# Performance work log

Measured on AMD Instinct MI355X. Metric: run time of the kernel, lower is better.

The kernel has to match this reference:

```python
import jax, jax.numpy as jnp
import numpy as np

EMB = 1024
HEADS = 16
HEAD_DIM = EMB // HEADS


def setup_inputs() -> dict:
    key = jax.random.key(0)
    ks = jax.random.split(key, 9)
    B, T = 2, 2048
    s = 1.0 / np.sqrt(EMB)
    x = jax.random.normal(ks[0], (B, T, EMB), dtype=jnp.float32)
    Wq = jax.random.normal(ks[1], (EMB, EMB), dtype=jnp.float32) * s
    bq = jnp.zeros((EMB,), dtype=jnp.float32)
    Wk = jax.random.normal(ks[2], (EMB, EMB), dtype=jnp.float32) * s
    bk = jnp.zeros((EMB,), dtype=jnp.float32)
    Wv = jax.random.normal(ks[3], (EMB, EMB), dtype=jnp.float32) * s
    bv = jnp.zeros((EMB,), dtype=jnp.float32)
    Wo = jax.random.normal(ks[4], (EMB, EMB), dtype=jnp.float32) * s
    bo = jnp.zeros((EMB,), dtype=jnp.float32)
    return {"x": x, "Wq": Wq, "bq": bq, "Wk": Wk, "bk": bk,
            "Wv": Wv, "bv": bv, "Wo": Wo, "bo": bo}


def reference(x, Wq, bq, Wk, bk, Wv, bv, Wo, bo):
    B, T, C = x.shape
    H, D = HEADS, HEAD_DIM
    # QKV projections -> (B, H, T, D)
    q = (x @ Wq + bq).reshape(B, T, H, D).transpose(0, 2, 1, 3)
    k = (x @ Wk + bk).reshape(B, T, H, D).transpose(0, 2, 1, 3)
    v = (x @ Wv + bv).reshape(B, T, H, D).transpose(0, 2, 1, 3)
    scores = jnp.einsum('bhqd,bhkd->bhqk', q, k) / np.sqrt(D).astype(np.float32)
    causal = jnp.tril(jnp.ones((T, T), dtype=bool))  # True where allowed
    scores = jnp.where(causal, scores, -jnp.inf)
    weights = jax.nn.softmax(scores, axis=-1)  # dropout is identity at eval
    out = jnp.einsum('bhqk,bhkd->bhqd', weights, v)
    out = out.transpose(0, 2, 1, 3).reshape(B, T, C)
    return out @ Wo + bo
```

## Files before the change

### kernel.cpp

```cpp
#include <hip/hip_runtime.h>

typedef unsigned short u16;
typedef u16 u16x8 __attribute__((ext_vector_type(8)));
typedef __bf16 bf16x8 __attribute__((ext_vector_type(8)));
typedef float f32x4 __attribute__((ext_vector_type(4)));

#define EMB 1024
#define TT 2048
#define BB 2
#define NHEADS 16
#define HD 64
#define MTOT (BB * TT)

__device__ __forceinline__ u16 cvt(float f) {
  return __builtin_bit_cast(u16, (__bf16)f);
}

__device__ __forceinline__ bf16x8 asbf(u16x8 v) {
  return __builtin_bit_cast(bf16x8, v);
}

__device__ __forceinline__ void gload16(const void* g, void* l) {
  __builtin_amdgcn_global_load_lds(
      (const __attribute__((address_space(1))) void*)g,
      (__attribute__((address_space(3))) void*)l, 16, 0, 0);
}

__global__ __launch_bounds__(256) void k_prep(
    const float* __restrict__ x, u16* __restrict__ xb,
    const float* __restrict__ W0, const float* __restrict__ W1,
    const float* __restrict__ W2, const float* __restrict__ W3,
    u16* __restrict__ T0, u16* __restrict__ T1, u16* __restrict__ T2,
    u16* __restrict__ T3) {
  __shared__ float tile[32][33];
  const int bid = blockIdx.x;
  const int tid = threadIdx.x;
  if (bid >= 4096) {
    int i = (bid - 4096) * 256 + tid;
    float4 a = ((const float4*)x)[i * 2];
    float4 b = ((const float4*)x)[i * 2 + 1];
    u16x8 o;
    o[0] = cvt(a.x); o[1] = cvt(a.y); o[2] = cvt(a.z); o[3] = cvt(a.w);
    o[4] = cvt(b.x); o[5] = cvt(b.y); o[6] = cvt(b.z); o[7] = cvt(b.w);
    ((u16x8*)xb)[i] = o;
    return;
  }
  const int z = bid >> 10;
  const float* __restrict__ W = (z == 0) ? W0 : (z == 1) ? W1 : (z == 2) ? W2 : W3;
  u16* __restrict__ Wt = (z == 0) ? T0 : (z == 1) ? T1 : (z == 2) ? T2 : T3;
  const int b = bid & 1023;
  const int bx = (b & 31) * 32, by = (b >> 5) * 32;
  const int tx = tid & 31;
  const int ty = tid >> 5;
#pragma unroll
  for (int r = ty; r < 32; r += 8) tile[r][tx] = W[(by + r) * EMB + bx + tx];
  __syncthreads();
  const int tx2 = tid & 15;
  const int ty2 = tid >> 4;
#pragma unroll
  for (int r = ty2; r < 32; r += 16) {
    unsigned v = (unsigned)cvt(tile[2 * tx2][r]) |
                 ((unsigned)cvt(tile[2 * tx2 + 1][r]) << 16);
    *(unsigned*)&Wt[(bx + r) * EMB + by + 2 * tx2] = v;
  }
}

__global__ __launch_bounds__(256) void k_gemm_qkv(
    const u16* __restrict__ xb, const u16* __restrict__ WqT,
    const u16* __restrict__ WkT, const u16* __restrict__ WvT,
    const float* __restrict__ bq, const float* __restrict__ bk,
    const float* __restrict__ bv, u16* __restrict__ Q, u16* __restrict__ K,
    u16* __restrict__ Vt) {
  __shared__ u16 WS[4][2][2][2048];
  const int tid = threadIdx.x;
  const int lane = tid & 63;
  const int w = tid >> 6;
  const int wr = w >> 1, wc = w & 1;
  const int lr = lane & 15, lg = lane >> 4;
  const int m0 = blockIdx.x * 128;
  const int nb = blockIdx.y;
  const int seg = nb >> 3;
  const int n0 = (nb & 7) * 128;
  const u16* __restrict__ Bt = (seg == 0) ? WqT : (seg == 1) ? WkT : WvT;
  const float* __restrict__ bias = (seg == 0) ? bq : (seg == 1) ? bk : bv;

  f32x4 acc[4][4];
#pragma unroll
  for (int i = 0; i < 4; i++)
#pragma unroll
    for (int j = 0; j < 4; j++) acc[i][j] = (f32x4){0.f, 0.f, 0.f, 0.f};

  const int srow = lane >> 2;
  const int sc = (lane & 3) ^ ((lane >> 3) & 3);
  const u16* gA = xb + (m0 + wr * 64 + srow) * EMB + sc * 8;
  const u16* gB = Bt + (n0 + wc * 64 + srow) * EMB + sc * 8;
  char* wbase = (char*)WS + w * 16384;
  const int pc = (lg ^ ((lr >> 1) & 3)) * 16;

#pragma unroll
  for (int j = 0; j < 4; j++) {
    gload16(gA + j * 16 * EMB, wbase + j * 1024);
    gload16(gB + j * 16 * EMB, wbase + 4096 + j * 1024);
  }

  for (int k0 = 0; k0 < EMB; k0 += 32) {
    const int cur = (k0 >> 5) & 1;
    char* bcur = wbase + cur * 8192;
    if (k0 + 32 < EMB) {
      char* bnxt = wbase + (cur ^ 1) * 8192;
      const int kn = k0 + 32;
#pragma unroll
      for (int j = 0; j < 4; j++) {
        gload16(gA + j * 16 * EMB + kn, bnxt + j * 1024);
        gload16(gB + j * 16 * EMB + kn, bnxt + 4096 + j * 1024);
      }
      asm volatile("s_waitcnt vmcnt(8)" ::: "memory");
    } else {
      asm volatile("s_waitcnt vmcnt(0)" ::: "memory");
    }
    __builtin_amdgcn_sched_barrier(0);
    u16x8 af[4], bf[4];
#pragma unroll
    for (int mi = 0; mi < 4; mi++)
      af[mi] = *(const u16x8*)(bcur + (mi * 16 + lr) * 64 + pc);
#pragma unroll
    for (int ni = 0; ni < 4; ni++)
      bf[ni] = *(const u16x8*)(bcur + 4096 + (ni * 16 + lr) * 64 + pc);
    __builtin_amdgcn_s_setprio(1);
#pragma unroll
    for (int mi = 0; mi < 4; mi++)
#pragma unroll
      for (int ni = 0; ni < 4; ni++)
        acc[mi][ni] = __builtin_amdgcn_mfma_f32_16x16x32_bf16(
            asbf(af[mi]), asbf(bf[ni]), acc[mi][ni], 0, 0, 0);
    __builtin_amdgcn_s_setprio(0);
  }

  const int b = m0 >> 11;
  if (seg == 2) {
#pragma unroll
    for (int ni = 0; ni < 4; ni++) {
      const int n = n0 + wc * 64 + ni * 16 + lr;
      const float bv_ = bias[n];
      const int h = n >> 6, d = n & 63;
      u16* vrow = Vt + (((b * NHEADS + h) * HD) + d) * TT;
#pragma unroll
      for (int mi = 0; mi < 4; mi++) {
        const int t0 = (m0 + wr * 64 + mi * 16 + lg * 4) & 2047;
        ushort4 pk;
        pk.x = cvt(acc[mi][ni][0] + bv_);
        pk.y = cvt(acc[mi][ni][1] + bv_);
        pk.z = cvt(acc[mi][ni][2] + bv_);
        pk.w = cvt(acc[mi][ni][3] + bv_);
        *(ushort4*)&vrow[t0] = pk;
      }
    }
  } else {
    u16* __restrict__ dst = (seg == 0) ? Q : K;
    const float qs = (seg == 0) ? 0.18033688011f : 1.0f;
#pragma unroll
    for (int mi = 0; mi < 4; mi++) {
      const int lmb = wr * 64 + mi * 16 + lg * 4;
#pragma unroll
      for (int ni = 0; ni < 4; ni++) {
        const int n = n0 + wc * 64 + ni * 16 + lr;
        const float bv_ = bias[n];
        const int h = n >> 6, d = n & 63;
#pragma unroll
        for (int r = 0; r < 4; r++) {
          const int t = (m0 + lmb + r) & 2047;
          float v = (acc[mi][ni][r] + bv_) * qs;
          dst[(((b * NHEADS + h) * TT) + t) * HD + d] = cvt(v);
        }
      }
    }
  }
}

__global__ __launch_bounds__(512) void k_attn(const u16* __restrict__ Q,
                                              const u16* __restrict__ Kg,
                                              const u16* __restrict__ Vt,
                                              u16* __restrict__ AO) {
  __shared__ u16 Kl[2][64 * 64];
  __shared__ u16 Vl[2][64 * 64];
  const int tid = threadIdx.x;
  const int lane = tid & 63;
  const int w = tid >> 6;
  const int lr = lane & 15, lg = lane >> 4;
  const int bh = blockIdx.x;
  const int pair = blockIdx.y;
  const int lo = pair, hi = 31 - pair;
  const int qblk = (w < 4) ? hi : lo;
  const int myend = qblk;
  const int q0 = qblk * 64 + (w & 3) * 16;
  const u16* __restrict__ Qh = Q + bh * TT * HD;
  const u16* __restrict__ Kh = Kg + bh * TT * HD;
  const u16* __restrict__ Vh = Vt + bh * HD * TT;

  const int srow = tid >> 3;
  const int sgz = ((tid >> 3) & 3) | (((tid >> 6) & 1) << 2);
  const int sc = (tid & 7) ^ sgz;

  u16x8 qf[2];
  qf[0] = *(const u16x8*)&Qh[(q0 + lr) * HD + lg * 8];
  qf[1] = *(const u16x8*)&Qh[(q0 + lr) * HD + 32 + lg * 8];

  f32x4 accO[4];
#pragma unroll
  for (int i = 0; i < 4; i++) accO[i] = (f32x4){0.f, 0.f, 0.f, 0.f};
  float mst = -__builtin_inff();
  float lsum = 0.f;

  const int nkt = hi + 1;

  gload16(Kh + srow * HD + sc * 8, (char*)Kl[0] + w * 1024);
  gload16(Vh + srow * TT + sc * 8, (char*)Vl[0] + w * 1024);
  __syncthreads();

  for (int kt = 0; kt < nkt; ++kt) {
    const int k0 = kt * 64;
    const int cur = kt & 1;
    if (kt + 1 < nkt) {
      const int kn = k0 + 64;
      gload16(Kh + (kn + srow) * HD + sc * 8, (char*)Kl[cur ^ 1] + w * 1024);
      gload16(Vh + srow * TT + kn + sc * 8, (char*)Vl[cur ^ 1] + w * 1024);
    }
    if (kt <= myend) {
      const char* Kc = (const char*)Kl[cur];
      const char* Vc = (const char*)Vl[cur];

      f32x4 s[4];
#pragma unroll
      for (int n = 0; n < 4; n++) s[n] = (f32x4){0.f, 0.f, 0.f, 0.f};
      __builtin_amdgcn_s_setprio(1);
#pragma unroll
      for (int n = 0; n < 4; n++) {
        const int kr =
            (lr & 3) + ((n & 1) << 2) + ((lr >> 2) << 3) + ((n >> 1) << 5);
        const int gg = (kr & 3) | (((kr >> 3) & 1) << 2);
#pragma unroll
        for (int dh = 0; dh < 2; dh++) {
          const int bo = ((dh * 4 + lg) ^ gg) << 4;
          u16x8 kf = *(const u16x8*)(Kc + kr * 128 + bo);
          s[n] = __builtin_amdgcn_mfma_f32_16x16x32_bf16(asbf(kf), asbf(qf[dh]),
                                                         s[n], 0, 0, 0);
        }
      }
      __builtin_amdgcn_s_setprio(0);
      if (kt == myend) {
        const int rowq = q0 + lr;
#pragma unroll
        for (int n = 0; n < 4; n++) {
          const int cb = k0 + ((n & 1) << 2) + (lg << 3) + ((n >> 1) << 5);
#pragma unroll
          for (int r = 0; r < 4; r++)
            if (cb + r > rowq) s[n][r] = -__builtin_inff();
        }
      }
      float m01 = fmaxf(fmaxf(s[0][0], s[0][1]), fmaxf(s[0][2], s[0][3]));
      float m1 = fmaxf(fmaxf(s[1][0], s[1][1]), fmaxf(s[1][2], s[1][3]));
      float m2 = fmaxf(fmaxf(s[2][0], s[2][1]), fmaxf(s[2][2], s[2][3]));
      float m3 = fmaxf(fmaxf(s[3][0], s[3][1]), fmaxf(s[3][2], s[3][3]));
      float lmax = fmaxf(fmaxf(m01, m1), fmaxf(m2, m3));
      if (!__all(lmax - mst <= 11.0f)) {
        float rm = lmax;
        rm = fmaxf(rm, __shfl_xor(rm, 16));
        rm = fmaxf(rm, __shfl_xor(rm, 32));
        float mnew = fmaxf(mst, rm);
        float corr = exp2f(mst - mnew);
        lsum *= corr;
        mst = mnew;
#pragma unroll
        for (int r = 0; r < 4; r++) {
          float ca = __shfl(corr, 20 * lg + r);
#pragma unroll
          for (int dt = 0; dt < 4; dt++) accO[dt][r] *= ca;
        }
      }
      float p[4][4];
      float ls = 0.f;
#pragma unroll
      for (int n = 0; n < 4; n++)
#pragma unroll
        for (int r = 0; r < 4; r++) {
          p[n][r] = exp2f(s[n][r] - mst);
          ls += p[n][r];
        }
      lsum += ls;
      u16x8 a1, a2;
#pragma unroll
      for (int r = 0; r < 4; r++) {
        a1[r] = cvt(p[0][r]);
        a1[4 + r] = cvt(p[1][r]);
        a2[r] = cvt(p[2][r]);
        a2[4 + r] = cvt(p[3][r]);
      }
      __builtin_amdgcn_s_setprio(1);
#pragma unroll
      for (int dt = 0; dt < 4; dt++) {
        const int row = dt * 16 + lr;
        const int gg = (row & 3) | (((row >> 3) & 1) << 2);
        const int bo0 = ((lg ^ gg) << 4);
        const int bo1 = (((4 + lg) ^ gg) << 4);
        u16x8 vf0 = *(const u16x8*)(Vc + row * 128 + bo0);
        u16x8 vf1 = *(const u16x8*)(Vc + row * 128 + bo1);
        accO[dt] = __builtin_amdgcn_mfma_f32_16x16x32_bf16(asbf(a1), asbf(vf0),
                                                           accO[dt], 0, 0, 0);
        accO[dt] = __builtin_amdgcn_mfma_f32_16x16x32_bf16(asbf(a2), asbf(vf1),
                                                           accO[dt], 0, 0, 0);
      }
      __builtin_amdgcn_s_setprio(0);
    }
    __syncthreads();
  }
  float t = lsum;
  t += __shfl_xor(t, 16);
  t += __shfl_xor(t, 32);
  float rinv = 1.0f / t;
  float ra[4];
#pragma unroll
  for (int r = 0; r < 4; r++) ra[r] = __shfl(rinv, 20 * lg + r);
  const int b = bh >> 4, h = bh & 15;
#pragma unroll
  for (int dt = 0; dt < 4; dt++)
#pragma unroll
    for (int r = 0; r < 4; r++) {
      const int row = q0 + lg * 4 + r;
      const int d = h * 64 + dt * 16 + lr;
      AO[(b * TT + row) * EMB + d] = cvt(accO[dt][r] * ra[r]);
    }
}

__global__ __launch_bounds__(256) void k_gemm_out(const u16* __restrict__ AO,
                                                  const u16* __restrict__ WoT,
                                                  const float* __restrict__ bo,
                                                  float* __restrict__ out) {
  __shared__ u16 Al[128 * 64];
  __shared__ u16 Bl[128 * 64];
  const int tid = threadIdx.x;
  const int lane = tid & 63;
  const int w = tid >> 6;
  const int wr = w >> 1, wc = w & 1;
  const int lr = lane & 15, lg = lane >> 4;
  const int m0 = blockIdx.x * 128;
  const int n0 = blockIdx.y * 128;

  f32x4 acc[4][4];
#pragma unroll
  for (int i = 0; i < 4; i++)
#pragma unroll
    for (int j = 0; j < 4; j++) acc[i][j] = (f32x4){0.f, 0.f, 0.f, 0.f};

  const int srow = tid >> 3;
  const int sgz = ((tid >> 3) & 3) | (((tid >> 6) & 1) << 2);
  const int sc = (tid & 7) ^ sgz;
  const u16* ga0 = AO + (m0 + srow) * EMB + sc * 8;
  const u16* gb0 = WoT + (n0 + srow) * EMB + sc * 8;
  char* la0 = (char*)Al + w * 1024;
  char* lb0 = (char*)Bl + w * 1024;
  const int gfr = (lr & 3) | (((lr >> 3) & 1) << 2);

  for (int k0 = 0; k0 < EMB; k0 += 64) {
#pragma unroll
    for (int m = 0; m < 4; m++) {
      gload16(ga0 + (32 * m) * EMB + k0, la0 + m * 4096);
      gload16(gb0 + (32 * m) * EMB + k0, lb0 + m * 4096);
    }
    __syncthreads();
    u16x8 af[4][2], bfr[4][2];
#pragma unroll
    for (int hh = 0; hh < 2; hh++) {
      const int pc = ((hh * 4 + lg) ^ gfr) * 16;
#pragma unroll
      for (int mi = 0; mi < 4; mi++)
        af[mi][hh] =
            *(const u16x8*)((char*)Al + (wr * 64 + mi * 16 + lr) * 128 + pc);
#pragma unroll
      for (int ni = 0; ni < 4; ni++)
        bfr[ni][hh] =
            *(const u16x8*)((char*)Bl + (wc * 64 + ni * 16 + lr) * 128 + pc);
    }
#pragma unroll
    for (int hh = 0; hh < 2; hh++)
#pragma unroll
      for (int mi = 0; mi < 4; mi++)
#pragma unroll
        for (int ni = 0; ni < 4; ni++)
          acc[mi][ni] = __builtin_amdgcn_mfma_f32_16x16x32_bf16(
              asbf(bfr[ni][hh]), asbf(af[mi][hh]), acc[mi][ni], 0, 0, 0);
    __syncthreads();
  }

#pragma unroll
  for (int ni = 0; ni < 4; ni++) {
    const int nbase = n0 + wc * 64 + ni * 16 + lg * 4;
    const float4 bv4 = *(const float4*)&bo[nbase];
#pragma unroll
    for (int mi = 0; mi < 4; mi++) {
      const int m = m0 + wr * 64 + mi * 16 + lr;
      float4 v;
      v.x = acc[mi][ni][0] + bv4.x;
      v.y = acc[mi][ni][1] + bv4.y;
      v.z = acc[mi][ni][2] + bv4.z;
      v.w = acc[mi][ni][3] + bv4.w;
      *(float4*)&out[m * EMB + nbase] = v;
    }
  }
}

extern "C" void kernel_launch(void* const* d_in, const int* in_sizes, int n_in,
                              void* d_out, int out_size, void* d_ws,
                              size_t ws_size, hipStream_t stream) {
  const float* x = (const float*)d_in[0];
  const float* Wq = (const float*)d_in[1];
  const float* bq = (const float*)d_in[2];
  const float* Wk = (const float*)d_in[3];
  const float* bk = (const float*)d_in[4];
  const float* Wv = (const float*)d_in[5];
  const float* bv = (const float*)d_in[6];
  const float* Wo = (const float*)d_in[7];
  const float* bo = (const float*)d_in[8];
  float* out = (float*)d_out;

  char* ws = (char*)d_ws;
  u16* xb = (u16*)ws;
  u16* WqT = (u16*)(ws + (8u << 20));
  u16* WkT = (u16*)(ws + (10u << 20));
  u16* WvT = (u16*)(ws + (12u << 20));
  u16* WoT = (u16*)(ws + (14u << 20));
  u16* Qb = (u16*)(ws + (16u << 20));
  u16* Kb = (u16*)(ws + (24u << 20));
  u16* Vtb = (u16*)(ws + (32u << 20));
  u16* AO = xb;

  k_prep<<<6144, 256, 0, stream>>>(x, xb, Wq, Wk, Wv, Wo, WqT, WkT, WvT, WoT);
  k_gemm_qkv<<<dim3(32, 24), 256, 0, stream>>>(xb, WqT, WkT, WvT, bq, bk, bv,
                                               Qb, Kb, Vtb);
  k_attn<<<dim3(32, 16), 512, 0, stream>>>(Qb, Kb, Vtb, AO);
  k_gemm_out<<<dim3(32, 8), 256, 0, stream>>>(AO, WoT, bo, out);
}
```

Baseline: 117.1 us.

## Load QKV GEMM operands directly from global into registers, dropping LDS staging

The QKV projection GEMM no longer stages A and B tiles through LDS with global_load_lds double buffering. Each lane now loads its MFMA fragments straight from global memory into registers, with register double buffering across two k-substeps. This removes the LDS traffic and its wait logic, but loses cross-wave reuse: each wave now fetches its own operands from global/L2, and the access pattern is strided per lane.

```diff
diff --git a/kernel.cpp b/kernel.cpp
--- a/kernel.cpp
+++ b/kernel.cpp
@@ -71,7 +71,6 @@
     const float* __restrict__ bq, const float* __restrict__ bk,
     const float* __restrict__ bv, u16* __restrict__ Q, u16* __restrict__ K,
     u16* __restrict__ Vt) {
-  __shared__ u16 WS[4][2][2][2048];
   const int tid = threadIdx.x;
   const int lane = tid & 63;
   const int w = tid >> 6;
@@ -90,49 +89,50 @@
 #pragma unroll
     for (int j = 0; j < 4; j++) acc[i][j] = (f32x4){0.f, 0.f, 0.f, 0.f};
 
-  const int srow = lane >> 2;
-  const int sc = (lane & 3) ^ ((lane >> 3) & 3);
-  const u16* gA = xb + (m0 + wr * 64 + srow) * EMB + sc * 8;
-  const u16* gB = Bt + (n0 + wc * 64 + srow) * EMB + sc * 8;
-  char* wbase = (char*)WS + w * 16384;
-  const int pc = (lg ^ ((lr >> 1) & 3)) * 16;
-
-#pragma unroll
-  for (int j = 0; j < 4; j++) {
-    gload16(gA + j * 16 * EMB, wbase + j * 1024);
-    gload16(gB + j * 16 * EMB, wbase + 4096 + j * 1024);
-  }
-
-  for (int k0 = 0; k0 < EMB; k0 += 32) {
-    const int cur = (k0 >> 5) & 1;
-    char* bcur = wbase + cur * 8192;
-    if (k0 + 32 < EMB) {
-      char* bnxt = wbase + (cur ^ 1) * 8192;
-      const int kn = k0 + 32;
-#pragma unroll
-      for (int j = 0; j < 4; j++) {
-        gload16(gA + j * 16 * EMB + kn, bnxt + j * 1024);
-        gload16(gB + j * 16 * EMB + kn, bnxt + 4096 + j * 1024);
-      }
-      asm volatile("s_waitcnt vmcnt(8)" ::: "memory");
-    } else {
-      asm volatile("s_waitcnt vmcnt(0)" ::: "memory");
-    }
-    __builtin_amdgcn_sched_barrier(0);
-    u16x8 af[4], bf[4];
-#pragma unroll
-    for (int mi = 0; mi < 4; mi++)
-      af[mi] = *(const u16x8*)(bcur + (mi * 16 + lr) * 64 + pc);
-#pragma unroll
-    for (int ni = 0; ni < 4; ni++)
-      bf[ni] = *(const u16x8*)(bcur + 4096 + (ni * 16 + lr) * 64 + pc);
+  const u16* aR[4];
+  const u16* bR[4];
+#pragma unroll
+  for (int mi = 0; mi < 4; mi++)
+    aR[mi] = xb + (m0 + wr * 64 + mi * 16 + lr) * EMB + lg * 8;
+#pragma unroll
+  for (int ni = 0; ni < 4; ni++)
+    bR[ni] = Bt + (n0 + wc * 64 + ni * 16 + lr) * EMB + lg * 8;
+
+  u16x8 a0[4], b0[4], a1[4], b1[4];
+#pragma unroll
+  for (int i = 0; i < 4; i++) {
+    a0[i] = *(const u16x8*)(aR[i]);
+    b0[i] = *(const u16x8*)(bR[i]);
+  }
+
+  for (int k0 = 0; k0 < EMB; k0 += 64) {
+#pragma unroll
+    for (int i = 0; i < 4; i++) {
+      a1[i] = *(const u16x8*)(aR[i] + k0 + 32);
+      b1[i] = *(const u16x8*)(bR[i] + k0 + 32);
+    }
     __builtin_amdgcn_s_setprio(1);
 #pragma unroll
     for (int mi = 0; mi < 4; mi++)
 #pragma unroll
       for (int ni = 0; ni < 4; ni++)
         acc[mi][ni] = __builtin_amdgcn_mfma_f32_16x16x32_bf16(
-            asbf(af[mi]), asbf(bf[ni]), acc[mi][ni], 0, 0, 0);
+            asbf(a0[mi]), asbf(b0[ni]), acc[mi][ni], 0, 0, 0);
+    __builtin_amdgcn_s_setprio(0);
+    if (k0 + 64 < EMB) {
+#pragma unroll
+      for (int i = 0; i < 4; i++) {
+        a0[i] = *(const u16x8*)(aR[i] + k0 + 64);
+        b0[i] = *(const u16x8*)(bR[i] + k0 + 64);
+      }
+    }
+    __builtin_amdgcn_s_setprio(1);
+#pragma unroll
+    for (int mi = 0; mi < 4; mi++)
+#pragma unroll
+      for (int ni = 0; ni < 4; ni++)
+        acc[mi][ni] = __builtin_amdgcn_mfma_f32_16x16x32_bf16(
+            asbf(a1[mi]), asbf(b1[ni]), acc[mi][ni], 0, 0, 0);
     __builtin_amdgcn_s_setprio(0);
   }
 
```

After: 161.3 us. +37.7%, slower.

## Use 256x256 block-shared tiles with 4-stage cp.async pipeline in QKV GEMM

Applied to the files above, without the earlier changes.

The QKV projection GEMM switches from 128x128 tiles with per-wave private double-buffered LDS to 256x256 tiles shared by 8 waves. It uses a 4-deep LDS ring with 3 stages in flight and a block barrier each k-step. Each wave computes a 128x64 sub-tile, so every loaded element is reused more and global traffic drops. In exchange the grid shrinks to 192 blocks on a 256-CU device, so some CUs sit idle. The kernel also adds a barrier per k-step and needs more registers for 32 accumulators.

```diff
diff --git a/kernel.cpp b/kernel.cpp
--- a/kernel.cpp
+++ b/kernel.cpp
@@ -65,70 +65,78 @@
   }
 }
 
-__global__ __launch_bounds__(256) void k_gemm_qkv(
+__global__ __launch_bounds__(512) void k_gemm_qkv(
     const u16* __restrict__ xb, const u16* __restrict__ WqT,
     const u16* __restrict__ WkT, const u16* __restrict__ WvT,
     const float* __restrict__ bq, const float* __restrict__ bk,
     const float* __restrict__ bv, u16* __restrict__ Q, u16* __restrict__ K,
     u16* __restrict__ Vt) {
-  __shared__ u16 WS[4][2][2][2048];
+  __shared__ u16 Al[4][256 * 32];
+  __shared__ u16 Bl[4][256 * 32];
   const int tid = threadIdx.x;
   const int lane = tid & 63;
   const int w = tid >> 6;
-  const int wr = w >> 1, wc = w & 1;
+  const int wm = w >> 2;
+  const int wn = w & 3;
   const int lr = lane & 15, lg = lane >> 4;
-  const int m0 = blockIdx.x * 128;
+  const int m0 = blockIdx.x * 256;
   const int nb = blockIdx.y;
-  const int seg = nb >> 3;
-  const int n0 = (nb & 7) * 128;
+  const int seg = nb >> 2;
+  const int n0 = (nb & 3) * 256;
   const u16* __restrict__ Bt = (seg == 0) ? WqT : (seg == 1) ? WkT : WvT;
   const float* __restrict__ bias = (seg == 0) ? bq : (seg == 1) ? bk : bv;
 
-  f32x4 acc[4][4];
-#pragma unroll
-  for (int i = 0; i < 4; i++)
+  f32x4 acc[8][4];
+#pragma unroll
+  for (int i = 0; i < 8; i++)
 #pragma unroll
     for (int j = 0; j < 4; j++) acc[i][j] = (f32x4){0.f, 0.f, 0.f, 0.f};
 
-  const int srow = lane >> 2;
-  const int sc = (lane & 3) ^ ((lane >> 3) & 3);
-  const u16* gA = xb + (m0 + wr * 64 + srow) * EMB + sc * 8;
-  const u16* gB = Bt + (n0 + wc * 64 + srow) * EMB + sc * 8;
-  char* wbase = (char*)WS + w * 16384;
+  const int sr0 = tid >> 2;
+  const int sc2 = (tid & 3) ^ ((tid >> 3) & 3);
+  const u16* gA = xb + (m0 + sr0) * EMB + sc2 * 8;
+  const u16* gB = Bt + (n0 + sr0) * EMB + sc2 * 8;
   const int pc = (lg ^ ((lr >> 1) & 3)) * 16;
 
-#pragma unroll
-  for (int j = 0; j < 4; j++) {
-    gload16(gA + j * 16 * EMB, wbase + j * 1024);
-    gload16(gB + j * 16 * EMB, wbase + 4096 + j * 1024);
-  }
-
-  for (int k0 = 0; k0 < EMB; k0 += 32) {
-    const int cur = (k0 >> 5) & 1;
-    char* bcur = wbase + cur * 8192;
-    if (k0 + 32 < EMB) {
-      char* bnxt = wbase + (cur ^ 1) * 8192;
-      const int kn = k0 + 32;
-#pragma unroll
-      for (int j = 0; j < 4; j++) {
-        gload16(gA + j * 16 * EMB + kn, bnxt + j * 1024);
-        gload16(gB + j * 16 * EMB + kn, bnxt + 4096 + j * 1024);
-      }
+  const int NK = 32;
+
+#pragma unroll
+  for (int s = 0; s < 3; s++) {
+    const int ka = s * 32;
+    gload16(gA + ka, (char*)Al[s] + w * 1024);
+    gload16(gA + 128 * EMB + ka, (char*)Al[s] + 8192 + w * 1024);
+    gload16(gB + ka, (char*)Bl[s] + w * 1024);
+    gload16(gB + 128 * EMB + ka, (char*)Bl[s] + 8192 + w * 1024);
+  }
+
+  for (int t = 0; t < NK; ++t) {
+    if (t <= NK - 3)
       asm volatile("s_waitcnt vmcnt(8)" ::: "memory");
-    } else {
+    else if (t == NK - 2)
+      asm volatile("s_waitcnt vmcnt(4)" ::: "memory");
+    else
       asm volatile("s_waitcnt vmcnt(0)" ::: "memory");
-    }
-    __builtin_amdgcn_sched_barrier(0);
-    u16x8 af[4], bf[4];
-#pragma unroll
-    for (int mi = 0; mi < 4; mi++)
-      af[mi] = *(const u16x8*)(bcur + (mi * 16 + lr) * 64 + pc);
+    __builtin_amdgcn_s_barrier();
+    if (t + 3 < NK) {
+      const int q = (t + 3) & 3;
+      const int ka = (t + 3) * 32;
+      gload16(gA + ka, (char*)Al[q] + w * 1024);
+      gload16(gA + 128 * EMB + ka, (char*)Al[q] + 8192 + w * 1024);
+      gload16(gB + ka, (char*)Bl[q] + w * 1024);
+      gload16(gB + 128 * EMB + ka, (char*)Bl[q] + 8192 + w * 1024);
+    }
+    const char* Ac = (const char*)Al[t & 3];
+    const char* Bc = (const char*)Bl[t & 3];
+    u16x8 af[8], bf[4];
 #pragma unroll
     for (int ni = 0; ni < 4; ni++)
-      bf[ni] = *(const u16x8*)(bcur + 4096 + (ni * 16 + lr) * 64 + pc);
+      bf[ni] = *(const u16x8*)(Bc + (wn * 64 + ni * 16 + lr) * 64 + pc);
+#pragma unroll
+    for (int mi = 0; mi < 8; mi++)
+      af[mi] = *(const u16x8*)(Ac + (wm * 128 + mi * 16 + lr) * 64 + pc);
     __builtin_amdgcn_s_setprio(1);
 #pragma unroll
-    for (int mi = 0; mi < 4; mi++)
+    for (int mi = 0; mi < 8; mi++)
 #pragma unroll
       for (int ni = 0; ni < 4; ni++)
         acc[mi][ni] = __builtin_amdgcn_mfma_f32_16x16x32_bf16(
@@ -140,13 +148,13 @@
   if (seg == 2) {
 #pragma unroll
     for (int ni = 0; ni < 4; ni++) {
-      const int n = n0 + wc * 64 + ni * 16 + lr;
+      const int n = n0 + wn * 64 + ni * 16 + lr;
       const float bv_ = bias[n];
       const int h = n >> 6, d = n & 63;
       u16* vrow = Vt + (((b * NHEADS + h) * HD) + d) * TT;
 #pragma unroll
-      for (int mi = 0; mi < 4; mi++) {
-        const int t0 = (m0 + wr * 64 + mi * 16 + lg * 4) & 2047;
+      for (int mi = 0; mi < 8; mi++) {
+        const int t0 = (m0 + wm * 128 + mi * 16 + lg * 4) & 2047;
         ushort4 pk;
         pk.x = cvt(acc[mi][ni][0] + bv_);
         pk.y = cvt(acc[mi][ni][1] + bv_);
@@ -159,11 +167,11 @@
     u16* __restrict__ dst = (seg == 0) ? Q : K;
     const float qs = (seg == 0) ? 0.18033688011f : 1.0f;
 #pragma unroll
-    for (int mi = 0; mi < 4; mi++) {
-      const int lmb = wr * 64 + mi * 16 + lg * 4;
+    for (int mi = 0; mi < 8; mi++) {
+      const int lmb = wm * 128 + mi * 16 + lg * 4;
 #pragma unroll
       for (int ni = 0; ni < 4; ni++) {
-        const int n = n0 + wc * 64 + ni * 16 + lr;
+        const int n = n0 + wn * 64 + ni * 16 + lr;
         const float bv_ = bias[n];
         const int h = n >> 6, d = n & 63;
 #pragma unroll
@@ -434,7 +442,7 @@
   u16* AO = xb;
 
   k_prep<<<6144, 256, 0, stream>>>(x, xb, Wq, Wk, Wv, Wo, WqT, WkT, WvT, WoT);
-  k_gemm_qkv<<<dim3(32, 24), 256, 0, stream>>>(xb, WqT, WkT, WvT, bq, bk, bv,
+  k_gemm_qkv<<<dim3(16, 12), 512, 0, stream>>>(xb, WqT, WkT, WvT, bq, bk, bv,
                                                Qb, Kb, Vtb);
   k_attn<<<dim3(32, 16), 512, 0, stream>>>(Qb, Kb, Vtb, AO);
   k_gemm_out<<<dim3(32, 8), 256, 0, stream>>>(AO, WoT, bo, out);
```

Result: slower. 120.0 us (+2.4%).
